# Optimization experiments

Hardware: AMD Instinct MI355X
Metric: run time of the kernel (lower is better)

Reference implementation:

```python
import jax, jax.numpy as jnp
import numpy as np
import math

NBITS = (1, 2, 4, 8)
S, B, D, H, F = 1024, 8, 1024, 16, 4096
HD = D // H


def _quant(w, nbit):
    """Symmetric uniform weight quantization to `nbit` bits with STE."""
    if nbit == 1:
        q = jnp.sign(w) * jnp.mean(jnp.abs(w))
    else:
        qmax = float(2 ** (nbit - 1) - 1)
        scale = jnp.max(jnp.abs(w)) / qmax
        q = jnp.clip(jnp.round(w / scale), -qmax - 1.0, qmax) * scale
    # straight-through estimator: forward uses q, backward flows through w
    return w + jax.lax.stop_gradient(q - w)


def _layernorm(x, g, b, eps=1e-5):
    m = jnp.mean(x, axis=-1, keepdims=True)
    v = jnp.var(x, axis=-1, keepdims=True)
    return (x - m) * jax.lax.rsqrt(v + eps) * g + b


def _quant_attn(src, w_in, b_in, w_out, b_out, nbit):
    # src: [S,B,D]; w_in: [3D,D]; w_out: [D,D]
    w_in_q = _quant(w_in, nbit)
    w_out_q = _quant(w_out, nbit)
    qkv = jnp.einsum('sbd,ed->sbe', src, w_in_q) + b_in  # [S,B,3D]
    q, k, v = jnp.split(qkv, 3, axis=-1)
    q = q.reshape(S, B, H, HD)
    k = k.reshape(S, B, H, HD)
    v = v.reshape(S, B, H, HD)
    scores = jnp.einsum('sbhd,tbhd->bhst', q, k) * (1.0 / math.sqrt(HD))
    p = jax.nn.softmax(scores, axis=-1)  # [B,H,S,S]
    o = jnp.einsum('bhst,tbhd->sbhd', p, v).reshape(S, B, D)
    return jnp.einsum('sbd,ed->sbe', o, w_out_q) + b_out


def setup_inputs() -> dict:
    key = jax.random.key(0)
    ks = jax.random.split(key, 12)
    sc = 0.02
    return {
        'src': jax.random.normal(ks[0], (S, B, D), jnp.float32),
        'alpha': jax.random.normal(ks[1], (3, 4), jnp.float32),
        'in_proj_w': jax.random.normal(ks[2], (4, 3 * D, D), jnp.float32) * sc,
        'in_proj_b': jnp.zeros((4, 3 * D), jnp.float32),
        'out_proj_w': jax.random.normal(ks[3], (4, D, D), jnp.float32) * sc,
        'out_proj_b': jnp.zeros((4, D), jnp.float32),
        'w1': jax.random.normal(ks[4], (4, F, D), jnp.float32) * sc,
        'b1': jnp.zeros((4, F), jnp.float32),
        'w2': jax.random.normal(ks[5], (4, D, F), jnp.float32) * sc,
        'b2': jnp.zeros((4, D), jnp.float32),
        'g1': jnp.ones((D,), jnp.float32),
        'be1': jnp.zeros((D,), jnp.float32),
        'g2': jnp.ones((D,), jnp.float32),
        'be2': jnp.zeros((D,), jnp.float32),
    }


def reference(src, alpha, in_proj_w, in_proj_b, out_proj_w, out_proj_b,
              w1, b1, w2, b2, g1, be1, g2, be2):
    probs = jax.nn.softmax(alpha, axis=-1)  # [3,4]
    # softmax-weighted mixture of multi-bitwidth attention branches
    src2 = jnp.zeros_like(src)
    for i, nbit in enumerate(NBITS):
        src2 = src2 + probs[0, i] * _quant_attn(
            src, in_proj_w[i], in_proj_b[i], out_proj_w[i], out_proj_b[i], nbit)
    x = _layernorm(src + src2, g1, be1)
    # mixture of quantized linear1 branches, then GELU
    h = jnp.zeros((S, B, F), src.dtype)
    for i, nbit in enumerate(NBITS):
        h = h + probs[1, i] * (jnp.einsum('sbd,fd->sbf', x, _quant(w1[i], nbit)) + b1[i])
    h = jax.nn.gelu(h, approximate=False)
    # mixture of quantized linear2 branches
    y = jnp.zeros_like(x)
    for i, nbit in enumerate(NBITS):
        y = y + probs[2, i] * (jnp.einsum('sbf,df->sbd', h, _quant(w2[i], nbit)) + b2[i])
    return _layernorm(x + y, g2, be2)
```

## Files before the change

kernel.cpp:

```cpp
#include <hip/hip_runtime.h>
#include <hip/hip_bf16.h>

typedef __attribute__((ext_vector_type(8))) unsigned short u16x8;
typedef __attribute__((ext_vector_type(4))) unsigned short u16x4;
typedef __attribute__((ext_vector_type(4))) int            i32x4;
typedef __attribute__((ext_vector_type(8))) __bf16         bf16x8;
typedef __attribute__((ext_vector_type(4))) float          f32x4;

#define SS 1024
#define BB 8
#define DD 1024
#define HH 16
#define HDD 64
#define FF 4096
#define MM 8192

#define GL16(g, l) __builtin_amdgcn_global_load_lds( \
    (__attribute__((address_space(1))) const void*)(g), \
    (__attribute__((address_space(3))) void*)(l), 16, 0, 0)

__device__ __forceinline__ float bf2f(unsigned short u) {
    return __uint_as_float(((unsigned int)u) << 16);
}
__device__ __forceinline__ unsigned short f2bf(float f) {
    unsigned int u = __float_as_uint(f);
    unsigned int r = (u + 0x7fffu + ((u >> 16) & 1u)) >> 16;
    return (unsigned short)r;
}
__device__ __forceinline__ float quantv(float w, float som, float qm) {
    if (qm == 0.f) {
        float sgn = (w > 0.f) ? 1.f : ((w < 0.f) ? -1.f : 0.f);
        return sgn * som;
    }
    if (som == 0.f) return 0.f;
    float q = rintf(w / som);
    q = fminf(fmaxf(q, -qm - 1.f), qm);
    return q * som;
}

__global__ __launch_bounds__(256) void k_stats(const float* __restrict__ w_in, const float* __restrict__ w_out,
                                               const float* __restrict__ w1, const float* __restrict__ w2,
                                               const float* __restrict__ src,
                                               float* __restrict__ pmax, float* __restrict__ psum) {
    const int t = blockIdx.y, blk = blockIdx.x, tid = threadIdx.x;
    const float* base; int n;
    if (t < 4)       { base = w_in  + (size_t)t * 3145728;     n = 3145728; }
    else if (t < 8)  { base = w_out + (size_t)(t-4) * 1048576; n = 1048576; }
    else if (t < 12) { base = w1    + (size_t)(t-8) * 4194304; n = 4194304; }
    else if (t < 16) { base = w2    + (size_t)(t-12) * 4194304; n = 4194304; }
    else             { base = src;                             n = 8388608; }
    const int n4 = n >> 2;
    float vmax = 0.f, vsum = 0.f;
    for (int i = blk * 256 + tid; i < n4; i += 65536) {
        float4 v = reinterpret_cast<const float4*>(base)[i];
        float a0 = fabsf(v.x), a1 = fabsf(v.y), a2 = fabsf(v.z), a3 = fabsf(v.w);
        vmax = fmaxf(vmax, fmaxf(fmaxf(a0, a1), fmaxf(a2, a3)));
        vsum += (a0 + a1) + (a2 + a3);
    }
#pragma unroll
    for (int m = 1; m < 64; m <<= 1) { vmax = fmaxf(vmax, __shfl_xor(vmax, m, 64)); vsum += __shfl_xor(vsum, m, 64); }
    __shared__ float sm[4], su[4];
    const int wave = tid >> 6, lane = tid & 63;
    if (lane == 0) { sm[wave] = vmax; su[wave] = vsum; }
    __syncthreads();
    if (tid == 0) {
        pmax[t * 256 + blk] = fmaxf(fmaxf(sm[0], sm[1]), fmaxf(sm[2], sm[3]));
        psum[t * 256 + blk] = (su[0] + su[1]) + (su[2] + su[3]);
    }
}

__global__ __launch_bounds__(256) void k_params(const float* __restrict__ pmax, const float* __restrict__ psum,
                                                const float* __restrict__ alpha, float* __restrict__ P) {
    __shared__ float rm[256], rs[256];
    const int tid = threadIdx.x;
    for (int t = 0; t < 17; ++t) {
        rm[tid] = pmax[t * 256 + tid];
        rs[tid] = psum[t * 256 + tid];
        __syncthreads();
        for (int s = 128; s > 0; s >>= 1) {
            if (tid < s) { rm[tid] = fmaxf(rm[tid], rm[tid + s]); rs[tid] += rs[tid + s]; }
            __syncthreads();
        }
        if (tid == 0) {
            if (t == 16) {
                P[50] = rm[0] * (1.f / 127.f);
            } else {
                const int nbits[4] = {1, 2, 4, 8};
                const int nb = nbits[t & 3];
                float nsize = (t < 4) ? 3145728.f : ((t < 8) ? 1048576.f : 4194304.f);
                if (nb == 1) { P[16 + 2*t] = rs[0] / nsize; P[17 + 2*t] = 0.f; }
                else { float qm = (float)((1 << (nb - 1)) - 1); P[16 + 2*t] = rm[0] / qm; P[17 + 2*t] = qm; }
            }
        }
        __syncthreads();
    }
    if (tid < 3) {
        float a[4], mx = -1e30f;
#pragma unroll
        for (int i = 0; i < 4; ++i) { a[i] = alpha[tid * 4 + i]; mx = fmaxf(mx, a[i]); }
        float e[4], ssum = 0.f;
#pragma unroll
        for (int i = 0; i < 4; ++i) { e[i] = expf(a[i] - mx); ssum += e[i]; }
#pragma unroll
        for (int i = 0; i < 4; ++i) P[tid * 4 + i] = e[i] / ssum;
    }
}

__global__ __launch_bounds__(256) void k_rmax(const float* __restrict__ part, int n, float* __restrict__ out) {
    const int tid = threadIdx.x;
    float m = 0.f;
    for (int i = tid; i < n; i += 256) m = fmaxf(m, part[i]);
#pragma unroll
    for (int s = 1; s < 64; s <<= 1) m = fmaxf(m, __shfl_xor(m, s, 64));
    __shared__ float sm[4];
    const int wave = tid >> 6, lane = tid & 63;
    if (lane == 0) sm[wave] = m;
    __syncthreads();
    if (tid == 0) *out = fmaxf(fmaxf(sm[0], sm[1]), fmaxf(sm[2], sm[3]));
}

__global__ __launch_bounds__(256) void k_quant8(const float* __restrict__ w, signed char* __restrict__ out,
                                                const float* __restrict__ P, int per_tensor, int tbase, int ntot) {
    int i = blockIdx.x * 256 + threadIdx.x;
    if (i >= ntot) return;
    int t = tbase + i / per_tensor;
    float som = P[16 + 2*t], qm = P[17 + 2*t];
    float v;
    float x = w[i];
    if (qm == 0.f)      v = (x > 0.f) ? 1.f : ((x < 0.f) ? -1.f : 0.f);
    else if (som == 0.f) v = 0.f;
    else                v = fminf(fmaxf(rintf(x / som), -qm - 1.f), qm);
    out[i] = (signed char)(int)v;
}

__global__ __launch_bounds__(256) void k_si8(const float* __restrict__ in, signed char* __restrict__ out,
                                             const float* __restrict__ P, int n4) {
    int i = blockIdx.x * 256 + threadIdx.x;
    if (i >= n4) return;
    const float sa = P[50];
    const float inv = (sa > 0.f) ? 1.f / sa : 0.f;
    float4 v = reinterpret_cast<const float4*>(in)[i];
    char4 o;
    o.x = (signed char)(int)fminf(fmaxf(rintf(v.x * inv), -127.f), 127.f);
    o.y = (signed char)(int)fminf(fmaxf(rintf(v.y * inv), -127.f), 127.f);
    o.z = (signed char)(int)fminf(fmaxf(rintf(v.z * inv), -127.f), 127.f);
    o.w = (signed char)(int)fminf(fmaxf(rintf(v.w * inv), -127.f), 127.f);
    reinterpret_cast<char4*>(out)[i] = o;
}

template <int NE, int MODE>
__global__ __launch_bounds__(256) void k_mixq8(const float* __restrict__ w, signed char* __restrict__ out,
                                               float* __restrict__ sB, const float* __restrict__ P,
                                               int tbase, int prow, size_t sz) {
    const int row = blockIdx.x, tid = threadIdx.x;
    const int L = NE * 256;
    float v[NE];
    float lm = 0.f;
#pragma unroll
    for (int j = 0; j < NE; ++j) {
        int k = j * 256 + tid;
        float acc;
        if (MODE == 0) {
            acc = 0.f;
#pragma unroll
            for (int br = 0; br < 4; ++br) {
                int t = tbase + br;
                acc += P[prow * 4 + br] * quantv(w[(size_t)br * sz + (size_t)row * L + k], P[16 + 2*t], P[17 + 2*t]);
            }
        } else {
            int i = k >> 10, e = k & 1023;
            int t = tbase + i;
            acc = P[i] * quantv(w[(size_t)i * sz + (size_t)row * 1024 + e], P[16 + 2*t], P[17 + 2*t]);
        }
        v[j] = acc;
        lm = fmaxf(lm, fabsf(acc));
    }
#pragma unroll
    for (int m = 1; m < 64; m <<= 1) lm = fmaxf(lm, __shfl_xor(lm, m, 64));
    __shared__ float sm[4];
    const int wave = tid >> 6, lane = tid & 63;
    if (lane == 0) sm[wave] = lm;
    __syncthreads();
    lm = fmaxf(fmaxf(sm[0], sm[1]), fmaxf(sm[2], sm[3]));
    if (tid == 0) sB[row] = lm * (1.f / 127.f);
    const float inv = (lm > 0.f) ? 127.f / lm : 0.f;
#pragma unroll
    for (int j = 0; j < NE; ++j)
        out[(size_t)row * L + j * 256 + tid] =
            (signed char)(int)fminf(fmaxf(rintf(v[j] * inv), -127.f), 127.f);
}

__global__ __launch_bounds__(256) void k_mixb(const float* __restrict__ b, float* __restrict__ out,
                                              const float* __restrict__ P, int prow, int n) {
    int i = blockIdx.x * 256 + threadIdx.x;
    if (i >= n) return;
    float acc = 0.f;
#pragma unroll
    for (int br = 0; br < 4; ++br) acc += P[prow * 4 + br] * b[(size_t)br * n + i];
    out[i] = acc;
}

__global__ __launch_bounds__(256) void k_q8(const unsigned short* __restrict__ in, signed char* __restrict__ out,
                                            const float* __restrict__ amax, int n8) {
    int i = blockIdx.x * 256 + threadIdx.x;
    if (i >= n8) return;
    const float am = *amax;
    const float inv = (am > 0.f) ? 127.f / am : 0.f;
    u16x8 v = reinterpret_cast<const u16x8*>(in)[i];
    union { signed char c[8]; unsigned long long u; } r;
#pragma unroll
    for (int e = 0; e < 8; ++e) {
        float f = bf2f(v[e]) * inv;
        r.c[e] = (signed char)(int)fminf(fmaxf(rintf(f), -127.f), 127.f);
    }
    reinterpret_cast<unsigned long long*>(out)[i] = r.u;
}

__global__ __launch_bounds__(256) void k_gemm_i8(const signed char* __restrict__ A,
                                                 const signed char* __restrict__ Bw,
                                                 unsigned short* __restrict__ C,
                                                 const float* __restrict__ bias,
                                                 const float* __restrict__ P, int tIdx,
                                                 int M, int N, int K, int XM, int XN) {
    const int gx = gridDim.x, gy = gridDim.y;
    const int flat = blockIdx.x + gx * blockIdx.y;
    const int xcd = flat & 7, r = flat >> 3;
    const int nloc = gx / XN, mloc = gy / XM;
    const int cm = xcd / XN, cn = xcd - cm * XN;
    const int by = cm * mloc + r / nloc;
    const int bx = cn * nloc + (r - (r / nloc) * nloc);

    __shared__ signed char As[2][128 * 128];
    __shared__ signed char Bs[2][128 * 128];
    const int tid = threadIdx.x;
    const int m0 = by * 128, n0 = bx * 128;
    const int lane = tid & 63, wave = tid >> 6;
    const int wr = wave >> 1, wc = wave & 1;
    const int lr = lane & 15, lg = lane >> 4;
    const int rsub = lane >> 3;
    const int csub = ((lane & 7) ^ rsub) * 16;
    const size_t aoff = (size_t)(m0 + rsub) * K + csub;
    const size_t boff = (size_t)(n0 + rsub) * K + csub;

    i32x4 acc[4][4];
#pragma unroll
    for (int m = 0; m < 4; ++m)
#pragma unroll
        for (int n = 0; n < 4; ++n) acc[m][n] = (i32x4){0, 0, 0, 0};

    auto stage = [&](int buf, int k0) {
#pragma unroll
        for (int it = 0; it < 4; ++it) {
            const int g = it * 4 + wave;
            GL16(A + aoff + (size_t)g * 8 * K + k0, &As[buf][g * 1024]);
            GL16(Bw + boff + (size_t)g * 8 * K + k0, &Bs[buf][g * 1024]);
        }
    };
    auto compute = [&](int buf) {
#pragma unroll
        for (int kh = 0; kh < 2; ++kh) {
            i32x4 af[4], bfr[4];
#pragma unroll
            for (int m = 0; m < 4; ++m) {
                int row = wr * 64 + m * 16 + lr;
                int cidx = (kh * 4 + lg) ^ (lr & 7);
                af[m] = *reinterpret_cast<const i32x4*>(&As[buf][row * 128 + cidx * 16]);
            }
#pragma unroll
            for (int n = 0; n < 4; ++n) {
                int row = wc * 64 + n * 16 + lr;
                int cidx = (kh * 4 + lg) ^ (lr & 7);
                bfr[n] = *reinterpret_cast<const i32x4*>(&Bs[buf][row * 128 + cidx * 16]);
            }
#pragma unroll
            for (int m = 0; m < 4; ++m)
#pragma unroll
                for (int n = 0; n < 4; ++n)
                    acc[m][n] = __builtin_amdgcn_mfma_i32_16x16x64_i8(
                        af[m], bfr[n], acc[m][n], 0, 0, 0);
        }
    };

    stage(0, 0);
    __syncthreads();
    int cur = 0;
    for (int k0 = 128; k0 < K; k0 += 128) {
        stage(cur ^ 1, k0);
        compute(cur);
        __syncthreads();
        cur ^= 1;
    }
    compute(cur);

    const float sab = P[50] * P[16 + 2 * tIdx];
#pragma unroll
    for (int n = 0; n < 4; ++n) {
        const int col = n0 + wc * 64 + n * 16 + lr;
        const float bv = bias[col];
#pragma unroll
        for (int m = 0; m < 4; ++m) {
#pragma unroll
            for (int j = 0; j < 4; ++j) {
                const int row = m0 + wr * 64 + m * 16 + lg * 4 + j;
                float v = (float)acc[m][n][j] * sab + bv;
                C[(size_t)row * N + col] = f2bf(v);
            }
        }
    }
}

__device__ __forceinline__ void store_out(float* C, size_t idx, float v) { C[idx] = v; }
__device__ __forceinline__ void store_out(unsigned short* C, size_t idx, float v) { C[idx] = f2bf(v); }

template <typename OutT, bool GELU>
__global__ __launch_bounds__(256) void k_gemm_i8s(const signed char* __restrict__ A,
                                                  const signed char* __restrict__ Bw,
                                                  OutT* __restrict__ C,
                                                  const float* __restrict__ bias,
                                                  const float* __restrict__ sB,
                                                  const float* __restrict__ aAm,
                                                  float* __restrict__ oPart,
                                                  int M, int N, int K, int XM, int XN) {
    const int gx = gridDim.x, gy = gridDim.y;
    const int flat = blockIdx.x + gx * blockIdx.y;
    const int xcd = flat & 7, r = flat >> 3;
    const int nloc = gx / XN, mloc = gy / XM;
    const int cm = xcd / XN, cn = xcd - cm * XN;
    const int by = cm * mloc + r / nloc;
    const int bx = cn * nloc + (r - (r / nloc) * nloc);

    __shared__ signed char As[2][128 * 128];
    __shared__ signed char Bs[2][128 * 128];
    __shared__ float smx[4];
    const int tid = threadIdx.x;
    const int m0 = by * 128, n0 = bx * 128;
    const int lane = tid & 63, wave = tid >> 6;
    const int wr = wave >> 1, wc = wave & 1;
    const int lr = lane & 15, lg = lane >> 4;
    const int rsub = lane >> 3;
    const int csub = ((lane & 7) ^ rsub) * 16;
    const size_t aoff = (size_t)(m0 + rsub) * K + csub;
    const size_t boff = (size_t)(n0 + rsub) * K + csub;

    i32x4 acc[4][4];
#pragma unroll
    for (int m = 0; m < 4; ++m)
#pragma unroll
        for (int n = 0; n < 4; ++n) acc[m][n] = (i32x4){0, 0, 0, 0};

    auto stage = [&](int buf, int k0) {
#pragma unroll
        for (int it = 0; it < 4; ++it) {
            const int g = it * 4 + wave;
            GL16(A + aoff + (size_t)g * 8 * K + k0, &As[buf][g * 1024]);
            GL16(Bw + boff + (size_t)g * 8 * K + k0, &Bs[buf][g * 1024]);
        }
    };
    auto compute = [&](int buf) {
#pragma unroll
        for (int kh = 0; kh < 2; ++kh) {
            i32x4 af[4], bfr[4];
#pragma unroll
            for (int m = 0; m < 4; ++m) {
                int row = wr * 64 + m * 16 + lr;
                int cidx = (kh * 4 + lg) ^ (lr & 7);
                af[m] = *reinterpret_cast<const i32x4*>(&As[buf][row * 128 + cidx * 16]);
            }
#pragma unroll
            for (int n = 0; n < 4; ++n) {
                int row = wc * 64 + n * 16 + lr;
                int cidx = (kh * 4 + lg) ^ (lr & 7);
                bfr[n] = *reinterpret_cast<const i32x4*>(&Bs[buf][row * 128 + cidx * 16]);
            }
#pragma unroll
            for (int m = 0; m < 4; ++m)
#pragma unroll
                for (int n = 0; n < 4; ++n)
                    acc[m][n] = __builtin_amdgcn_mfma_i32_16x16x64_i8(
                        af[m], bfr[n], acc[m][n], 0, 0, 0);
        }
    };

    stage(0, 0);
    __syncthreads();
    int cur = 0;
    for (int k0 = 128; k0 < K; k0 += 128) {
        stage(cur ^ 1, k0);
        compute(cur);
        __syncthreads();
        cur ^= 1;
    }
    compute(cur);

    const float sA = (*aAm) * (1.f / 127.f);
    float lm = 0.f;
#pragma unroll
    for (int n = 0; n < 4; ++n) {
        const int col = n0 + wc * 64 + n * 16 + lr;
        const float sc = sA * sB[col];
        const float bv = bias ? bias[col] : 0.f;
#pragma unroll
        for (int m = 0; m < 4; ++m) {
#pragma unroll
            for (int j = 0; j < 4; ++j) {
                const int row = m0 + wr * 64 + m * 16 + lg * 4 + j;
                float v = (float)acc[m][n][j] * sc + bv;
                if (GELU) v = 0.5f * v * (1.f + erff(v * 0.70710678118654752f));
                store_out(C, (size_t)row * N + col, v);
                if (oPart) lm = fmaxf(lm, fabsf(v));
            }
        }
    }
    if (oPart) {
#pragma unroll
        for (int m = 1; m < 64; m <<= 1) lm = fmaxf(lm, __shfl_xor(lm, m, 64));
        if (lane == 0) smx[wave] = lm;
        __syncthreads();
        if (tid == 0) oPart[flat] = fmaxf(fmaxf(smx[0], smx[1]), fmaxf(smx[2], smx[3]));
    }
}

__global__ __launch_bounds__(256) void k_fmfma(const unsigned short* __restrict__ qkvb, int qstride,
                                               unsigned short* __restrict__ outb, int ostride,
                                               float* __restrict__ oPart) {
    __shared__ unsigned short Ks[64 * 64];
    __shared__ unsigned short Vt[64 * 64];
    __shared__ unsigned short Pl[4 * 16 * 72];
    __shared__ float smx[4];
    const int tid = threadIdx.x;
    const int lane = tid & 63, wave = tid >> 6;
    const int lr = lane & 15, lg = lane >> 4;
    const int s0 = blockIdx.x * 64;
    const int bh = blockIdx.y;
    const int b = bh >> 4, hh = bh & 15;
    const int hb = hh * 64;

    u16x8 qf[2];
    {
        const size_t qb = (size_t)((s0 + wave * 16 + lr) * 8 + b) * qstride + hb;
#pragma unroll
        for (int ks = 0; ks < 2; ++ks)
            qf[ks] = *reinterpret_cast<const u16x8*>(qkvb + qb + ks * 32 + lg * 8);
    }
    float m_old = -1e30f, l_run = 0.f;
    f32x4 oacc[4];
#pragma unroll
    for (int n = 0; n < 4; ++n) oacc[n] = (f32x4){0.f, 0.f, 0.f, 0.f};
    unsigned short* myP = Pl + wave * (16 * 72);

    for (int kt = 0; kt < 16; ++kt) {
        __syncthreads();
#pragma unroll
        for (int it = 0; it < 2; ++it) {
            int c = tid + it * 256;
            int row = c >> 3, ch = c & 7;
            const size_t gb = (size_t)((kt * 64 + row) * 8 + b) * qstride + hb + ch * 8;
            int chs = ch ^ (row & 7);
            *reinterpret_cast<u16x8*>(&Ks[row * 64 + chs * 8]) =
                *reinterpret_cast<const u16x8*>(qkvb + gb + 1024);
            u16x8 vv = *reinterpret_cast<const u16x8*>(qkvb + gb + 2048);
            const int vbase = ((row >> 3) ^ ch) * 8 + (row & 7);
#pragma unroll
            for (int e = 0; e < 8; ++e) Vt[(ch * 8 + e) * 64 + vbase] = vv[e];
        }
        __syncthreads();
        f32x4 sacc[4];
#pragma unroll
        for (int n = 0; n < 4; ++n) sacc[n] = (f32x4){0.f, 0.f, 0.f, 0.f};
#pragma unroll
        for (int ks = 0; ks < 2; ++ks) {
#pragma unroll
            for (int n = 0; n < 4; ++n) {
                int row = n * 16 + lr;
                int cidx = (ks * 4 + lg) ^ (lr & 7);
                u16x8 kf = *reinterpret_cast<const u16x8*>(&Ks[row * 64 + cidx * 8]);
                sacc[n] = __builtin_amdgcn_mfma_f32_16x16x32_bf16(
                    __builtin_bit_cast(bf16x8, kf), __builtin_bit_cast(bf16x8, qf[ks]),
                    sacc[n], 0, 0, 0);
            }
        }
        float pmax = -1e30f;
#pragma unroll
        for (int n = 0; n < 4; ++n)
#pragma unroll
            for (int j = 0; j < 4; ++j) { sacc[n][j] *= 0.125f; pmax = fmaxf(pmax, sacc[n][j]); }
        pmax = fmaxf(pmax, __shfl_xor(pmax, 16, 64));
        pmax = fmaxf(pmax, __shfl_xor(pmax, 32, 64));
        const float m_new = fmaxf(m_old, pmax);
        const float corr = __expf(m_old - m_new);
        float pv[16];
        float psum = 0.f;
#pragma unroll
        for (int n = 0; n < 4; ++n)
#pragma unroll
            for (int j = 0; j < 4; ++j) { float e = __expf(sacc[n][j] - m_new); pv[n * 4 + j] = e; psum += e; }
        psum += __shfl_xor(psum, 16, 64);
        psum += __shfl_xor(psum, 32, 64);
        l_run = l_run * corr + psum;
        m_old = m_new;
#pragma unroll
        for (int n = 0; n < 4; ++n)
#pragma unroll
            for (int t2 = 0; t2 < 2; ++t2) {
                int key = n * 16 + lg * 4 + t2 * 2;
                unsigned int pk = (unsigned int)f2bf(pv[n * 4 + t2 * 2]) |
                                  ((unsigned int)f2bf(pv[n * 4 + t2 * 2 + 1]) << 16);
                *reinterpret_cast<unsigned int*>(&myP[lr * 72 + key]) = pk;
            }
#pragma unroll
        for (int j = 0; j < 4; ++j) {
            float cj = __shfl(corr, lg * 4 + j, 64);
#pragma unroll
            for (int n = 0; n < 4; ++n) oacc[n][j] *= cj;
        }
#pragma unroll
        for (int ks = 0; ks < 2; ++ks) {
            u16x8 pa = *reinterpret_cast<const u16x8*>(&myP[lr * 72 + ks * 32 + lg * 8]);
#pragma unroll
            for (int n = 0; n < 4; ++n) {
                int d = n * 16 + lr;
                int kcs = (ks * 4 + lg) ^ (d >> 3);
                u16x8 vf = *reinterpret_cast<const u16x8*>(&Vt[d * 64 + kcs * 8]);
                oacc[n] = __builtin_amdgcn_mfma_f32_16x16x32_bf16(
                    __builtin_bit_cast(bf16x8, pa), __builtin_bit_cast(bf16x8, vf),
                    oacc[n], 0, 0, 0);
            }
        }
    }
    const float linv = 1.f / l_run;
    float lm = 0.f;
#pragma unroll
    for (int j = 0; j < 4; ++j) {
        float lj = __shfl(linv, lg * 4 + j, 64);
        const size_t rowb = (size_t)((s0 + wave * 16 + lg * 4 + j) * 8 + b) * ostride + hb;
#pragma unroll
        for (int n = 0; n < 4; ++n) {
            float v = oacc[n][j] * lj;
            outb[rowb + n * 16 + lr] = f2bf(v);
            lm = fmaxf(lm, fabsf(v));
        }
    }
#pragma unroll
    for (int m = 1; m < 64; m <<= 1) lm = fmaxf(lm, __shfl_xor(lm, m, 64));
    if (lane == 0) smx[wave] = lm;
    __syncthreads();
    if (tid == 0) oPart[blockIdx.x + gridDim.x * blockIdx.y] =
        fmaxf(fmaxf(smx[0], smx[1]), fmaxf(smx[2], smx[3]));
}

__global__ __launch_bounds__(256) void k_ln(const float* __restrict__ xf, const unsigned short* __restrict__ xb,
                                            const float* __restrict__ r,
                                            const float* __restrict__ g, const float* __restrict__ be,
                                            float* __restrict__ outf, unsigned short* __restrict__ outb,
                                            float* __restrict__ oPart) {
    const int row = blockIdx.x, tid = threadIdx.x;
    const size_t base = (size_t)row * 1024 + tid * 4;
    float x0, x1, x2, x3;
    if (xf) {
        float4 xv = *reinterpret_cast<const float4*>(xf + base);
        x0 = xv.x; x1 = xv.y; x2 = xv.z; x3 = xv.w;
    } else {
        u16x4 xv = *reinterpret_cast<const u16x4*>(xb + base);
        x0 = bf2f(xv[0]); x1 = bf2f(xv[1]); x2 = bf2f(xv[2]); x3 = bf2f(xv[3]);
    }
    float4 rv = *reinterpret_cast<const float4*>(r + base);
    float t0 = x0 + rv.x, t1 = x1 + rv.y, t2 = x2 + rv.z, t3 = x3 + rv.w;
    float s = t0 + t1 + t2 + t3;
    float ss = t0 * t0 + t1 * t1 + t2 * t2 + t3 * t3;
#pragma unroll
    for (int m = 1; m < 64; m <<= 1) { s += __shfl_xor(s, m, 64); ss += __shfl_xor(ss, m, 64); }
    __shared__ float red[8];
    __shared__ float smx[4];
    const int wave = tid >> 6, lane = tid & 63;
    if (lane == 0) { red[wave] = s; red[4 + wave] = ss; }
    __syncthreads();
    s = red[0] + red[1] + red[2] + red[3];
    ss = red[4] + red[5] + red[6] + red[7];
    const float mean = s * (1.f / 1024.f);
    const float var = ss * (1.f / 1024.f) - mean * mean;
    const float rstd = rsqrtf(var + 1e-5f);
    float4 gv = *reinterpret_cast<const float4*>(g + tid * 4);
    float4 bv = *reinterpret_cast<const float4*>(be + tid * 4);
    float o0 = (t0 - mean) * rstd * gv.x + bv.x;
    float o1 = (t1 - mean) * rstd * gv.y + bv.y;
    float o2 = (t2 - mean) * rstd * gv.z + bv.z;
    float o3 = (t3 - mean) * rstd * gv.w + bv.w;
    if (outf) {
        float4 ov = {o0, o1, o2, o3};
        *reinterpret_cast<float4*>(outf + base) = ov;
    }
    if (outb) {
        u16x4 q; q[0] = f2bf(o0); q[1] = f2bf(o1); q[2] = f2bf(o2); q[3] = f2bf(o3);
        *reinterpret_cast<u16x4*>(outb + base) = q;
    }
    if (oPart) {
        float lm = fmaxf(fmaxf(fabsf(o0), fabsf(o1)), fmaxf(fabsf(o2), fabsf(o3)));
#pragma unroll
        for (int m = 1; m < 64; m <<= 1) lm = fmaxf(lm, __shfl_xor(lm, m, 64));
        if (lane == 0) smx[wave] = lm;
        __syncthreads();
        if (tid == 0) oPart[row] = fmaxf(fmaxf(smx[0], smx[1]), fmaxf(smx[2], smx[3]));
    }
}

extern "C" void kernel_launch(void* const* d_in, const int* in_sizes, int n_in,
                              void* d_out, int out_size, void* d_ws, size_t ws_size,
                              hipStream_t stream) {
    const float* src   = (const float*)d_in[0];
    const float* alpha = (const float*)d_in[1];
    const float* w_in  = (const float*)d_in[2];
    const float* b_in  = (const float*)d_in[3];
    const float* w_out = (const float*)d_in[4];
    const float* b_out = (const float*)d_in[5];
    const float* w1    = (const float*)d_in[6];
    const float* b1    = (const float*)d_in[7];
    const float* w2    = (const float*)d_in[8];
    const float* b2    = (const float*)d_in[9];
    const float* g1    = (const float*)d_in[10];
    const float* be1   = (const float*)d_in[11];
    const float* g2    = (const float*)d_in[12];
    const float* be2   = (const float*)d_in[13];

    char* ws = (char*)d_ws;
    size_t off = 0;
    auto alloc = [&](size_t bytes) { size_t r = off; off += (bytes + 255) & ~(size_t)255; return r; };
    float* P              = (float*)(ws + alloc(1024));
    float* amaxv          = (float*)(ws + alloc(256));
    float* flashPart      = (float*)(ws + alloc(8192 * 4));
    float* lnPart         = (float*)(ws + alloc(8192 * 4));
    float* hPart          = (float*)(ws + alloc(2048 * 4));
    float* pmax           = (float*)(ws + alloc(17 * 256 * 4));
    float* psum           = (float*)(ws + alloc(17 * 256 * 4));
    signed char* WinQ8    = (signed char*)(ws + alloc((size_t)4 * 3072 * 1024));
    signed char* WoutC8   = (signed char*)(ws + alloc((size_t)1024 * 4096));
    float* sOut           = (float*)(ws + alloc(1024 * 4));
    signed char* W1m8     = (signed char*)(ws + alloc((size_t)4096 * 1024));
    float* s1             = (float*)(ws + alloc(4096 * 4));
    signed char* W2m8     = (signed char*)(ws + alloc((size_t)1024 * 4096));
    float* s2             = (float*)(ws + alloc(1024 * 4));
    float* b1m            = (float*)(ws + alloc(4096 * 4));
    float* b2m            = (float*)(ws + alloc(1024 * 4));
    float* bOm            = (float*)(ws + alloc(1024 * 4));
    signed char* Si8      = (signed char*)(ws + alloc((size_t)MM * 1024));
    unsigned short* Xbf   = (unsigned short*)(ws + alloc((size_t)MM * 1024 * 2));
    signed char* Xi8      = (signed char*)(ws + alloc((size_t)MM * 1024));
    unsigned short* attnC = (unsigned short*)(ws + alloc((size_t)MM * 4096 * 2));
    unsigned short* qkvB  = (unsigned short*)(ws + alloc((size_t)MM * 3072 * 2));
    signed char* attnC8   = (signed char*)qkvB;
    unsigned short* h     = attnC;
    signed char* h8       = (signed char*)qkvB;
    if (ws_size < off) return;

    float* outF = (float*)d_out;

    k_stats<<<dim3(256, 17), 256, 0, stream>>>(w_in, w_out, w1, w2, src, pmax, psum);
    k_params<<<1, 256, 0, stream>>>(pmax, psum, alpha, P);
    {
        int n = 4 * 3072 * 1024;
        k_quant8<<<(n + 255) / 256, 256, 0, stream>>>(w_in, WinQ8, P, 3072 * 1024, 0, n);
        k_mixq8<16, 1><<<1024, 256, 0, stream>>>(w_out, WoutC8, sOut, P, 4, 0, 1048576);
        k_mixq8<4, 0><<<4096, 256, 0, stream>>>(w1, W1m8, s1, P, 8, 1, 4194304);
        k_mixq8<16, 0><<<1024, 256, 0, stream>>>(w2, W2m8, s2, P, 12, 2, 4194304);
        k_mixb<<<(4096 + 255) / 256, 256, 0, stream>>>(b1, b1m, P, 1, 4096);
        k_mixb<<<(1024 + 255) / 256, 256, 0, stream>>>(b2, b2m, P, 2, 1024);
        k_mixb<<<(1024 + 255) / 256, 256, 0, stream>>>(b_out, bOm, P, 0, 1024);
        k_si8<<<(2097152 + 255) / 256, 256, 0, stream>>>(src, Si8, P, 2097152);
    }
    for (int i = 0; i < 4; ++i) {
        k_gemm_i8<<<dim3(24, 64), 256, 0, stream>>>(
            Si8, WinQ8 + (size_t)i * 3072 * 1024, qkvB, b_in + i * 3072, P, i, MM, 3072, 1024, 1, 8);
        k_fmfma<<<dim3(16, 128), 256, 0, stream>>>(qkvB, 3072, attnC + i * 1024, 4096,
                                                   flashPart + i * 2048);
    }
    k_rmax<<<1, 256, 0, stream>>>(flashPart, 8192, amaxv + 0);
    k_q8<<<(4194304 + 255) / 256, 256, 0, stream>>>(attnC, attnC8, amaxv + 0, 4194304);
    k_gemm_i8s<float, false><<<dim3(8, 64), 256, 0, stream>>>(
        attnC8, WoutC8, outF, bOm, sOut, amaxv + 0, nullptr, MM, 1024, 4096, 4, 2);
    k_ln<<<MM, 256, 0, stream>>>(src, nullptr, outF, g1, be1, nullptr, Xbf, lnPart);
    k_rmax<<<1, 256, 0, stream>>>(lnPart, 8192, amaxv + 1);
    k_q8<<<(1048576 + 255) / 256, 256, 0, stream>>>(Xbf, Xi8, amaxv + 1, 1048576);
    k_gemm_i8s<unsigned short, true><<<dim3(32, 64), 256, 0, stream>>>(
        Xi8, W1m8, h, b1m, s1, amaxv + 1, hPart, MM, 4096, 1024, 1, 8);
    k_rmax<<<1, 256, 0, stream>>>(hPart, 2048, amaxv + 2);
    k_q8<<<(4194304 + 255) / 256, 256, 0, stream>>>(h, h8, amaxv + 2, 4194304);
    k_gemm_i8s<float, false><<<dim3(8, 64), 256, 0, stream>>>(
        h8, W2m8, outF, b2m, s2, amaxv + 2, nullptr, MM, 1024, 4096, 4, 2);
    k_ln<<<MM, 256, 0, stream>>>(nullptr, Xbf, outF, g2, be2, outF, nullptr, nullptr);
}
```

Before: 977.6 us.

## Load K tiles via global_load_lds, swizzle V transpose, remap flash-attention grid

The flash-attention kernel now stages K tiles with direct global-to-LDS loads, using a per-lane XOR swizzle so MFMA reads stay bank-conflict free. The V transpose store gets an extra XOR term to spread LDS banks. The grid is flattened and remapped so consecutive blocks cover different batch/head pairs, which should improve L2 locality and load spread. bf16 conversion now uses a hardware cast instead of manual rounding, which could change NaN handling and rounding on edge values.

```diff
diff --git a/kernel.cpp b/kernel.cpp
--- a/kernel.cpp
+++ b/kernel.cpp
@@ -23,9 +23,7 @@
     return __uint_as_float(((unsigned int)u) << 16);
 }
 __device__ __forceinline__ unsigned short f2bf(float f) {
-    unsigned int u = __float_as_uint(f);
-    unsigned int r = (u + 0x7fffu + ((u >> 16) & 1u)) >> 16;
-    return (unsigned short)r;
+    return __builtin_bit_cast(unsigned short, (__bf16)f);
 }
 __device__ __forceinline__ float quantv(float w, float som, float qm) {
     if (qm == 0.f) {
@@ -430,8 +428,9 @@
     const int tid = threadIdx.x;
     const int lane = tid & 63, wave = tid >> 6;
     const int lr = lane & 15, lg = lane >> 4;
-    const int s0 = blockIdx.x * 64;
-    const int bh = blockIdx.y;
+    const int f = blockIdx.x;
+    const int bh = (f & 7) * 16 + (f >> 7);
+    const int s0 = ((f >> 3) & 15) * 64;
     const int b = bh >> 4, hh = bh & 15;
     const int hb = hh * 64;
 
@@ -442,6 +441,10 @@
         for (int ks = 0; ks < 2; ++ks)
             qf[ks] = *reinterpret_cast<const u16x8*>(qkvb + qb + ks * 32 + lg * 8);
     }
+    const int rsub = lane >> 3;
+    const int csub = ((lane & 7) ^ rsub) * 8;
+    const unsigned short* kS = qkvb + (size_t)(rsub * 8 + b) * qstride + 1024 + hb + csub;
+
     float m_old = -1e30f, l_run = 0.f;
     f32x4 oacc[4];
 #pragma unroll
@@ -450,18 +453,20 @@
 
     for (int kt = 0; kt < 16; ++kt) {
         __syncthreads();
+#pragma unroll
+        for (int it = 0; it < 2; ++it) {
+            const int g = it * 4 + wave;
+            GL16(kS + (size_t)((kt * 64 + g * 8) * 8) * qstride, &Ks[g * 512]);
+        }
 #pragma unroll
         for (int it = 0; it < 2; ++it) {
             int c = tid + it * 256;
             int row = c >> 3, ch = c & 7;
             const size_t gb = (size_t)((kt * 64 + row) * 8 + b) * qstride + hb + ch * 8;
-            int chs = ch ^ (row & 7);
-            *reinterpret_cast<u16x8*>(&Ks[row * 64 + chs * 8]) =
-                *reinterpret_cast<const u16x8*>(qkvb + gb + 1024);
             u16x8 vv = *reinterpret_cast<const u16x8*>(qkvb + gb + 2048);
             const int vbase = ((row >> 3) ^ ch) * 8 + (row & 7);
 #pragma unroll
-            for (int e = 0; e < 8; ++e) Vt[(ch * 8 + e) * 64 + vbase] = vv[e];
+            for (int e = 0; e < 8; ++e) Vt[(ch * 8 + e) * 64 + (vbase ^ (e * 8))] = vv[e];
         }
         __syncthreads();
         f32x4 sacc[4];
@@ -503,8 +508,9 @@
 #pragma unroll
             for (int t2 = 0; t2 < 2; ++t2) {
                 int key = n * 16 + lg * 4 + t2 * 2;
-                unsigned int pk = (unsigned int)f2bf(pv[n * 4 + t2 * 2]) |
-                                  ((unsigned int)f2bf(pv[n * 4 + t2 * 2 + 1]) << 16);
+                unsigned int pk =
+                    (unsigned int)__builtin_bit_cast(unsigned short, (__bf16)pv[n * 4 + t2 * 2]) |
+                    ((unsigned int)__builtin_bit_cast(unsigned short, (__bf16)pv[n * 4 + t2 * 2 + 1]) << 16);
                 *reinterpret_cast<unsigned int*>(&myP[lr * 72 + key]) = pk;
             }
 #pragma unroll
@@ -519,7 +525,7 @@
 #pragma unroll
             for (int n = 0; n < 4; ++n) {
                 int d = n * 16 + lr;
-                int kcs = (ks * 4 + lg) ^ (d >> 3);
+                int kcs = ((ks * 4 + lg) ^ (d >> 3)) ^ (d & 7);
                 u16x8 vf = *reinterpret_cast<const u16x8*>(&Vt[d * 64 + kcs * 8]);
                 oacc[n] = __builtin_amdgcn_mfma_f32_16x16x32_bf16(
                     __builtin_bit_cast(bf16x8, pa), __builtin_bit_cast(bf16x8, vf),
@@ -544,8 +550,7 @@
     for (int m = 1; m < 64; m <<= 1) lm = fmaxf(lm, __shfl_xor(lm, m, 64));
     if (lane == 0) smx[wave] = lm;
     __syncthreads();
-    if (tid == 0) oPart[blockIdx.x + gridDim.x * blockIdx.y] =
-        fmaxf(fmaxf(smx[0], smx[1]), fmaxf(smx[2], smx[3]));
+    if (tid == 0) oPart[f] = fmaxf(fmaxf(smx[0], smx[1]), fmaxf(smx[2], smx[3]));
 }
 
 __global__ __launch_bounds__(256) void k_ln(const float* __restrict__ xf, const unsigned short* __restrict__ xb,
@@ -669,8 +674,8 @@
     for (int i = 0; i < 4; ++i) {
         k_gemm_i8<<<dim3(24, 64), 256, 0, stream>>>(
             Si8, WinQ8 + (size_t)i * 3072 * 1024, qkvB, b_in + i * 3072, P, i, MM, 3072, 1024, 1, 8);
-        k_fmfma<<<dim3(16, 128), 256, 0, stream>>>(qkvB, 3072, attnC + i * 1024, 4096,
-                                                   flashPart + i * 2048);
+        k_fmfma<<<dim3(2048), 256, 0, stream>>>(qkvB, 3072, attnC + i * 1024, 4096,
+                                                flashPart + i * 2048);
     }
     k_rmax<<<1, 256, 0, stream>>>(flashPart, 8192, amaxv + 0);
     k_q8<<<(4194304 + 255) / 256, 256, 0, stream>>>(attnC, attnC8, amaxv + 0, 4194304);
```

Result: faster. 934.8 us (-4.4%).
